# Kernel optimization log

Measured on AMD Instinct MI355X. Metric: run time of the kernel, lower is better.

## Reference

```python
import jax, jax.numpy as jnp
import numpy as np

B, S, D, H = 8, 1024, 1024, 16
HD = D // H
EPS = 1e-06


def setup_inputs() -> dict:
    key = jax.random.key(0)
    ks = jax.random.split(key, 10)
    sc = 0.02
    inp = {
        "y": jax.random.normal(ks[0], (B, S, D), dtype=jnp.float32),
        "y_mask": jax.random.randint(ks[1], (B, 1, 1, S), 0, 2) == 1,
        "Wq": jax.random.normal(ks[2], (D, D), dtype=jnp.float32) * sc,
        "bq": jnp.zeros((D,), jnp.float32),
        "Wk": jax.random.normal(ks[3], (D, D), dtype=jnp.float32) * sc,
        "bk": jnp.zeros((D,), jnp.float32),
        "Wv": jax.random.normal(ks[4], (D, D), dtype=jnp.float32) * sc,
        "bv": jnp.zeros((D,), jnp.float32),
        "Wm": jax.random.normal(ks[5], (D, D), dtype=jnp.float32) * sc,
        "bm": jnp.zeros((D,), jnp.float32),
        "a2": jnp.ones((D,), jnp.float32),
        "b2": jnp.zeros((D,), jnp.float32),
    }
    return inp


def _heads(x):
    # [B,S,D] -> [B,H,S,HD]
    return x.reshape(B, S, H, HD).transpose(0, 2, 1, 3)


def reference(y, y_mask, Wq, bq, Wk, bk, Wv, bv, Wm, bm, a2, b2):
    # torch Linear: x @ W^T + b
    q = _heads(y @ Wq.T + bq)
    k = _heads(y @ Wk.T + bk)
    v = _heads(y @ Wv.T + bv)
    scores = jnp.einsum("bhqd,bhkd->bhqk", q, k) / jnp.sqrt(jnp.float32(HD))
    scores = jnp.where(y_mask, jnp.float32(-1e9), scores)
    att = jax.nn.softmax(scores, axis=-1)  # dropout = identity in eval
    atted = jnp.einsum("bhqk,bhkd->bhqd", att, v)
    atted = atted.transpose(0, 2, 1, 3).reshape(B, S, D)
    atted = atted @ Wm.T + bm
    x = y + atted  # residual (dropout1 = identity in eval)
    mean = x.mean(-1, keepdims=True)
    # torch std: unbiased (ddof=1); eps added to std, not variance
    std = jnp.sqrt(((x - mean) ** 2).sum(-1, keepdims=True) / jnp.float32(D - 1))
    return a2 * (x - mean) / (std + EPS) + b2
```

## Files before the change

### kernel.cpp

```cpp
#include <hip/hip_runtime.h>

#define DEVFN __device__ __forceinline__

typedef unsigned short u16;
typedef __attribute__((ext_vector_type(8))) unsigned short u16x8;
typedef __attribute__((ext_vector_type(4))) unsigned short u16x4;
typedef __attribute__((ext_vector_type(8))) __bf16 bf16x8;
typedef __attribute__((ext_vector_type(4))) float f32x4;

DEVFN u16 f2bf_hw(float f) {
    return __builtin_bit_cast(u16, (__bf16)f);
}

DEVFN float bf2f(u16 h) {
    unsigned u = (unsigned)h << 16;
    return __builtin_bit_cast(float, u);
}

DEVFN bf16x8 ldfrag(const u16* p) {
    return __builtin_bit_cast(bf16x8, *(const u16x8*)p);
}

DEVFN f32x4 mfma16(bf16x8 a, bf16x8 b, f32x4 c) {
    return __builtin_amdgcn_mfma_f32_16x16x32_bf16(a, b, c, 0, 0, 0);
}

DEVFN void async16(const u16* g, u16* l) {
    __builtin_amdgcn_global_load_lds(
        (const __attribute__((address_space(1))) void*)g,
        (__attribute__((address_space(3))) void*)l, 16, 0, 0);
}

__global__ __launch_bounds__(256) void conv_all(const float* __restrict__ y,
                                                const float* __restrict__ w0,
                                                const float* __restrict__ w1,
                                                const float* __restrict__ w2,
                                                const float* __restrict__ w3,
                                                u16* __restrict__ yb,
                                                u16* __restrict__ wb,
                                                const int* __restrict__ mask,
                                                int* __restrict__ idx,
                                                int* __restrict__ cnt) {
    const int b = blockIdx.x;
    if (b >= 12288) {
        const int wave = threadIdx.x >> 6, lane = threadIdx.x & 63;
        for (int bb = wave; bb < 8; bb += 4) {
            const int* m = mask + bb * 1024;
            int* ib = idx + bb * 1024;
            int base = 0;
            for (int t = 0; t < 16; ++t) {
                const int pos = t * 64 + lane;
                const int valid = (m[pos] == 0) ? 1 : 0;
                const unsigned long long bal = __ballot(valid);
                const int pre = __popcll(bal & ((1ull << lane) - 1ull));
                if (valid) ib[base + pre] = pos;
                base += (int)__popcll(bal);
            }
            if (lane == 0) cnt[bb] = base;
            for (int i = base + lane; i < 1024; i += 64) ib[i] = 0;
        }
        return;
    }
    const float* src;
    u16* dst;
    int i;
    if (b < 8192) {
        src = y; dst = yb;
        i = b * 1024 + threadIdx.x * 4;
    } else {
        const int g = (b - 8192) >> 10;
        src = g == 0 ? w0 : (g == 1 ? w1 : (g == 2 ? w2 : w3));
        dst = wb + (size_t)g * 1024 * 1024;
        i = ((b - 8192) & 1023) * 1024 + threadIdx.x * 4;
    }
    const float4 v = *(const float4*)&src[i];
    u16x4 o;
    o.x = f2bf_hw(v.x); o.y = f2bf_hw(v.y);
    o.z = f2bf_hw(v.z); o.w = f2bf_hw(v.w);
    *(u16x4*)&dst[i] = o;
}

__global__ __launch_bounds__(256, 4) void gemm_bt(const u16* __restrict__ A,
                                                  const u16* __restrict__ Bt,
                                                  const float* __restrict__ b0,
                                                  const float* __restrict__ b1,
                                                  const float* __restrict__ b2,
                                                  u16* __restrict__ C0,
                                                  u16* __restrict__ C1,
                                                  u16* __restrict__ C2,
                                                  int K) {
    __shared__ u16 lA[128 * 32];
    __shared__ u16 lB[128 * 32];
    const int tid = threadIdx.x;
    const int wave = tid >> 6, lane = tid & 63;
    const int quad = lane >> 4, l16 = lane & 15;
    const int n0 = blockIdx.x * 128, m0 = blockIdx.y * 128;
    const int wm = (wave >> 1) * 64, wn = (wave & 1) * 64;
    const int srow = tid >> 2, scol = (tid & 3) * 8;
    const u16* Ag0 = A + (size_t)(m0 + srow) * K + scol;
    const u16* Ag1 = A + (size_t)(m0 + 64 + srow) * K + scol;
    const u16* Bg0 = Bt + (size_t)(n0 + srow) * K + scol;
    const u16* Bg1 = Bt + (size_t)(n0 + 64 + srow) * K + scol;
    u16* lA0 = &lA[wave * 512];
    u16* lA1 = &lA[2048 + wave * 512];
    u16* lB0 = &lB[wave * 512];
    u16* lB1 = &lB[2048 + wave * 512];
    f32x4 acc[4][4] = {};
    for (int k0 = 0; k0 < K; k0 += 32) {
        __syncthreads();
        async16(Ag0 + k0, lA0);
        async16(Ag1 + k0, lA1);
        async16(Bg0 + k0, lB0);
        async16(Bg1 + k0, lB1);
        __syncthreads();
        bf16x8 af[4], bfr[4];
        #pragma unroll
        for (int i = 0; i < 4; ++i)
            af[i] = ldfrag(&lA[(wm + i * 16 + l16) * 32 + quad * 8]);
        #pragma unroll
        for (int i = 0; i < 4; ++i)
            bfr[i] = ldfrag(&lB[(wn + i * 16 + l16) * 32 + quad * 8]);
        #pragma unroll
        for (int mi = 0; mi < 4; ++mi)
            #pragma unroll
            for (int ni = 0; ni < 4; ++ni)
                acc[mi][ni] = mfma16(af[mi], bfr[ni], acc[mi][ni]);
    }
    #pragma unroll
    for (int mi = 0; mi < 4; ++mi) {
        #pragma unroll
        for (int ni = 0; ni < 4; ++ni) {
            const int col = n0 + wn + ni * 16 + l16;
            const int cs = col >> 10;
            const int c = col & 1023;
            const float* bp = cs == 0 ? b0 : (cs == 1 ? b1 : b2);
            u16* cp = cs == 0 ? C0 : (cs == 1 ? C1 : C2);
            const float bb = bp[c];
            #pragma unroll
            for (int r = 0; r < 4; ++r) {
                const int row = m0 + wm + mi * 16 + quad * 4 + r;
                cp[(size_t)row * 1024 + c] = f2bf_hw(acc[mi][ni][r] + bb);
            }
        }
    }
}

__global__ __launch_bounds__(256) void transpose_vc(const u16* __restrict__ v,
                                                    u16* __restrict__ vt,
                                                    const int* __restrict__ idx,
                                                    const int* __restrict__ cnt) {
    const int bh = blockIdx.y, bb = bh >> 4, h = bh & 15;
    const int s0 = blockIdx.x * 64;
    const int cn = cnt[bb];
    if (s0 >= ((cn + 63) & ~63)) return;
    __shared__ u16 t[64 * 72];
    const int r = threadIdx.x >> 3, c8 = (threadIdx.x & 7) * 8;
    #pragma unroll
    for (int rr = 0; rr < 64; rr += 32) {
        const int src = idx[bb * 1024 + s0 + r + rr];
        *(u16x8*)&t[(r + rr) * 72 + c8] =
            *(const u16x8*)&v[(size_t)(bb * 1024 + src) * 1024 + h * 64 + c8];
    }
    __syncthreads();
    #pragma unroll
    for (int rr = 0; rr < 64; rr += 32) {
        u16x8 o;
        #pragma unroll
        for (int j = 0; j < 8; ++j) o[j] = t[(c8 + j) * 72 + (r + rr)];
        *(u16x8*)&vt[(size_t)(bh * 64 + r + rr) * 1024 + s0 + c8] = o;
    }
}

__global__ __launch_bounds__(256) void attn(const u16* __restrict__ qb,
                                            const u16* __restrict__ kb,
                                            const u16* __restrict__ vtb,
                                            const int* __restrict__ idxb,
                                            const int* __restrict__ cntb,
                                            u16* __restrict__ attb) {
    const int lin = blockIdx.x;
    const int xcd = lin & 7, slot = lin >> 3;
    const int bh = xcd * 16 + (slot >> 3);
    const int q0 = (slot & 7) * 128;
    const int bb = bh >> 4, h = bh & 15;
    const int tid = threadIdx.x, wave = tid >> 6, lane = tid & 63;
    const int quad = lane >> 4, l16 = lane & 15;
    __shared__ u16 lK[64 * 72];
    __shared__ u16 lV[64 * 72];
    __shared__ u16 lP[128 * 72];

    const int cn = cntb[bb];
    const int kEnd = (cn + 63) & ~63;
    const int* ib = idxb + bb * 1024;

    bf16x8 aq[2][2];
    #pragma unroll
    for (int rg = 0; rg < 2; ++rg) {
        const int qrow = q0 + wave * 32 + rg * 16 + l16;
        const u16* qp = qb + (size_t)(bb * 1024 + qrow) * 1024 + h * 64 + quad * 8;
        aq[rg][0] = ldfrag(qp);
        aq[rg][1] = ldfrag(qp + 32);
    }

    f32x4 o[2][4] = {};
    float ps_acc[2][4] = {};

    const int srow = tid >> 3, scol = (tid & 7) * 8;
    const u16* kbase = kb + (size_t)(bb * 1024) * 1024 + h * 64 + scol;
    const u16* vbase = vtb + (size_t)(bh * 64 + srow) * 1024 + scol;

    int gi0 = ib[srow], gi1 = ib[srow + 32];
    u16x8 nk0 = *(const u16x8*)(kbase + (size_t)gi0 * 1024);
    u16x8 nk1 = *(const u16x8*)(kbase + (size_t)gi1 * 1024);
    u16x8 nv0 = *(const u16x8*)(vbase);
    u16x8 nv1 = *(const u16x8*)(vbase + (size_t)32 * 1024);

    const float C = 0.18033688011112043f;

    for (int kt = 0; kt < kEnd; kt += 64) {
        __syncthreads();
        *(u16x8*)&lK[srow * 72 + scol] = nk0;
        *(u16x8*)&lK[(srow + 32) * 72 + scol] = nk1;
        *(u16x8*)&lV[srow * 72 + scol] = nv0;
        *(u16x8*)&lV[(srow + 32) * 72 + scol] = nv1;
        __syncthreads();
        const int ktn = kt + 64;
        if (ktn < kEnd) {
            gi0 = ib[ktn + srow]; gi1 = ib[ktn + srow + 32];
            nk0 = *(const u16x8*)(kbase + (size_t)gi0 * 1024);
            nk1 = *(const u16x8*)(kbase + (size_t)gi1 * 1024);
            nv0 = *(const u16x8*)(vbase + ktn);
            nv1 = *(const u16x8*)(vbase + (size_t)32 * 1024 + ktn);
        }

        bf16x8 kf[4][2];
        #pragma unroll
        for (int n = 0; n < 4; ++n) {
            kf[n][0] = ldfrag(&lK[(n * 16 + l16) * 72 + quad * 8]);
            kf[n][1] = ldfrag(&lK[(n * 16 + l16) * 72 + 32 + quad * 8]);
        }
        f32x4 s[2][4];
        #pragma unroll
        for (int rg = 0; rg < 2; ++rg)
            #pragma unroll
            for (int n = 0; n < 4; ++n) {
                f32x4 t = {};
                t = mfma16(aq[rg][0], kf[n][0], t);
                t = mfma16(aq[rg][1], kf[n][1], t);
                s[rg][n] = t;
            }
        float bias[4];
        #pragma unroll
        for (int n = 0; n < 4; ++n)
            bias[n] = (kt + n * 16 + l16 < cn) ? 0.0f : -1e9f;
        #pragma unroll
        for (int rg = 0; rg < 2; ++rg)
            #pragma unroll
            for (int n = 0; n < 4; ++n)
                #pragma unroll
                for (int r = 0; r < 4; ++r) {
                    const float p =
                        __builtin_amdgcn_exp2f(__builtin_fmaf(s[rg][n][r], C, bias[n]));
                    ps_acc[rg][r] += p;
                    lP[(wave * 32 + rg * 16 + quad * 4 + r) * 72 + n * 16 + l16] =
                        f2bf_hw(p);
                }
        __asm__ __volatile__("s_waitcnt lgkmcnt(0)" ::: "memory");
        bf16x8 ap[2][2];
        #pragma unroll
        for (int rg = 0; rg < 2; ++rg) {
            ap[rg][0] = ldfrag(&lP[(wave * 32 + rg * 16 + l16) * 72 + quad * 8]);
            ap[rg][1] = ldfrag(&lP[(wave * 32 + rg * 16 + l16) * 72 + 32 + quad * 8]);
        }
        bf16x8 vf[4][2];
        #pragma unroll
        for (int ni = 0; ni < 4; ++ni) {
            vf[ni][0] = ldfrag(&lV[(ni * 16 + l16) * 72 + quad * 8]);
            vf[ni][1] = ldfrag(&lV[(ni * 16 + l16) * 72 + 32 + quad * 8]);
        }
        #pragma unroll
        for (int rg = 0; rg < 2; ++rg)
            #pragma unroll
            for (int ni = 0; ni < 4; ++ni) {
                o[rg][ni] = mfma16(ap[rg][0], vf[ni][0], o[rg][ni]);
                o[rg][ni] = mfma16(ap[rg][1], vf[ni][1], o[rg][ni]);
            }
    }
    #pragma unroll
    for (int off = 1; off < 16; off <<= 1)
        #pragma unroll
        for (int rg = 0; rg < 2; ++rg)
            #pragma unroll
            for (int r = 0; r < 4; ++r)
                ps_acc[rg][r] += __shfl_xor(ps_acc[rg][r], off);
    float rl[2][4];
    #pragma unroll
    for (int rg = 0; rg < 2; ++rg)
        #pragma unroll
        for (int r = 0; r < 4; ++r) rl[rg][r] = 1.f / ps_acc[rg][r];
    #pragma unroll
    for (int rg = 0; rg < 2; ++rg)
        #pragma unroll
        for (int ni = 0; ni < 4; ++ni)
            #pragma unroll
            for (int r = 0; r < 4; ++r) {
                const int row = q0 + wave * 32 + rg * 16 + quad * 4 + r;
                attb[(size_t)(bb * 1024 + row) * 1024 + h * 64 + ni * 16 + l16] =
                    f2bf_hw(o[rg][ni][r] * rl[rg][r]);
            }
}

__global__ __launch_bounds__(256) void ln_res(const float* __restrict__ y,
                                              const u16* __restrict__ xpb,
                                              const float* __restrict__ a2,
                                              const float* __restrict__ b2,
                                              float* __restrict__ out) {
    const int row = blockIdx.x, tid = threadIdx.x;
    const size_t base = (size_t)row * 1024;
    const int j = tid * 4;
    const float4 yv = *(const float4*)&y[base + j];
    const u16x4 xv = *(const u16x4*)&xpb[base + j];
    float x[4] = {yv.x + bf2f(xv.x), yv.y + bf2f(xv.y),
                  yv.z + bf2f(xv.z), yv.w + bf2f(xv.w)};
    float s = 0.f, ss = 0.f;
    #pragma unroll
    for (int i = 0; i < 4; ++i) { s += x[i]; ss += x[i] * x[i]; }
    #pragma unroll
    for (int off = 1; off < 64; off <<= 1) {
        s += __shfl_xor(s, off);
        ss += __shfl_xor(ss, off);
    }
    __shared__ float rs[4], rss[4];
    const int wave = tid >> 6, lane = tid & 63;
    if (lane == 0) { rs[wave] = s; rss[wave] = ss; }
    __syncthreads();
    s = rs[0] + rs[1] + rs[2] + rs[3];
    ss = rss[0] + rss[1] + rss[2] + rss[3];
    const float mean = s * (1.f / 1024.f);
    float var = (ss - s * mean) * (1.f / 1023.f);
    var = fmaxf(var, 0.f);
    const float inv = 1.f / (sqrtf(var) + 1e-6f);
    const float4 av = *(const float4*)&a2[j];
    const float4 bv = *(const float4*)&b2[j];
    float4 ov;
    ov.x = av.x * (x[0] - mean) * inv + bv.x;
    ov.y = av.y * (x[1] - mean) * inv + bv.y;
    ov.z = av.z * (x[2] - mean) * inv + bv.z;
    ov.w = av.w * (x[3] - mean) * inv + bv.w;
    *(float4*)&out[base + j] = ov;
}

extern "C" void kernel_launch(void* const* d_in, const int* in_sizes, int n_in,
                              void* d_out, int out_size, void* d_ws, size_t ws_size,
                              hipStream_t stream) {
    (void)in_sizes; (void)n_in; (void)out_size;
    const float* y   = (const float*)d_in[0];
    const int*   msk = (const int*)d_in[1];
    const float* Wq  = (const float*)d_in[2];
    const float* bq  = (const float*)d_in[3];
    const float* Wk  = (const float*)d_in[4];
    const float* bkb = (const float*)d_in[5];
    const float* Wv  = (const float*)d_in[6];
    const float* bv  = (const float*)d_in[7];
    const float* Wm  = (const float*)d_in[8];
    const float* bm  = (const float*)d_in[9];
    const float* a2  = (const float*)d_in[10];
    const float* b2  = (const float*)d_in[11];
    float* out = (float*)d_out;

    char* ws = (char*)d_ws;
    const size_t MB = 1u << 20;
    if (ws_size < 72 * MB) return;
    u16* yb  = (u16*)(ws);
    u16* wqb = (u16*)(ws + 16 * MB);
    u16* wmb = (u16*)(ws + 22 * MB);
    u16* qb  = (u16*)(ws + 24 * MB);
    u16* kb  = (u16*)(ws + 40 * MB);
    u16* vb  = (u16*)(ws + 56 * MB);
    u16* vtb  = yb;
    u16* attb = vb;
    u16* xpb  = qb;

    int* idxb = (int*)d_out;
    int* cntb = idxb + 8192;

    conv_all<<<12289, 256, 0, stream>>>(y, Wq, Wk, Wv, Wm, yb, wqb,
                                        msk, idxb, cntb);

    gemm_bt<<<dim3(24, 64), 256, 0, stream>>>(
        yb, wqb, bq, bkb, bv, qb, kb, vb, 1024);

    transpose_vc<<<dim3(16, 128), 256, 0, stream>>>(vb, vtb, idxb, cntb);
    attn<<<dim3(1024), 256, 0, stream>>>(qb, kb, vtb, idxb, cntb, attb);

    gemm_bt<<<dim3(8, 64), 256, 0, stream>>>(
        attb, wmb, bm, bm, bm, xpb, xpb, xpb, 1024);
    ln_res<<<8192, 256, 0, stream>>>(y, xpb, a2, b2, out);
}
```

Baseline: 278.1 us.

## Fuse V transpose into attention and split-K the output projection

Removes the standalone V gather/transpose kernel; attention now gathers V rows by index and transposes them into shared memory with scalar stores. The output projection GEMM is split into two K halves to double block count, writing two bf16 partials that the layernorm kernel sums. This trades a kernel launch and a V round-trip through memory for more LDS store work in attention, extra partial-buffer traffic and extra bf16 rounding.

```diff
diff --git a/kernel.cpp b/kernel.cpp
--- a/kernel.cpp
+++ b/kernel.cpp
@@ -88,19 +88,24 @@
                                                   u16* __restrict__ C0,
                                                   u16* __restrict__ C1,
                                                   u16* __restrict__ C2,
-                                                  int K) {
+                                                  u16* __restrict__ Calt,
+                                                  int K, int ld, int nx) {
     __shared__ u16 lA[128 * 32];
     __shared__ u16 lB[128 * 32];
     const int tid = threadIdx.x;
     const int wave = tid >> 6, lane = tid & 63;
     const int quad = lane >> 4, l16 = lane & 15;
-    const int n0 = blockIdx.x * 128, m0 = blockIdx.y * 128;
+    const int bx = blockIdx.x;
+    const int half = bx / nx;
+    const int n0 = (bx % nx) * 128, m0 = blockIdx.y * 128;
     const int wm = (wave >> 1) * 64, wn = (wave & 1) * 64;
     const int srow = tid >> 2, scol = (tid & 3) * 8;
-    const u16* Ag0 = A + (size_t)(m0 + srow) * K + scol;
-    const u16* Ag1 = A + (size_t)(m0 + 64 + srow) * K + scol;
-    const u16* Bg0 = Bt + (size_t)(n0 + srow) * K + scol;
-    const u16* Bg1 = Bt + (size_t)(n0 + 64 + srow) * K + scol;
+    const u16* Ab = A + half * K;
+    const u16* Bb = Bt + half * K;
+    const u16* Ag0 = Ab + (size_t)(m0 + srow) * ld + scol;
+    const u16* Ag1 = Ab + (size_t)(m0 + 64 + srow) * ld + scol;
+    const u16* Bg0 = Bb + (size_t)(n0 + srow) * ld + scol;
+    const u16* Bg1 = Bb + (size_t)(n0 + 64 + srow) * ld + scol;
     u16* lA0 = &lA[wave * 512];
     u16* lA1 = &lA[2048 + wave * 512];
     u16* lB0 = &lB[wave * 512];
@@ -134,8 +139,8 @@
             const int cs = col >> 10;
             const int c = col & 1023;
             const float* bp = cs == 0 ? b0 : (cs == 1 ? b1 : b2);
-            u16* cp = cs == 0 ? C0 : (cs == 1 ? C1 : C2);
-            const float bb = bp[c];
+            u16* cp = half ? Calt : (cs == 0 ? C0 : (cs == 1 ? C1 : C2));
+            const float bb = half ? 0.0f : bp[c];
             #pragma unroll
             for (int r = 0; r < 4; ++r) {
                 const int row = m0 + wm + mi * 16 + quad * 4 + r;
@@ -145,35 +150,9 @@
     }
 }
 
-__global__ __launch_bounds__(256) void transpose_vc(const u16* __restrict__ v,
-                                                    u16* __restrict__ vt,
-                                                    const int* __restrict__ idx,
-                                                    const int* __restrict__ cnt) {
-    const int bh = blockIdx.y, bb = bh >> 4, h = bh & 15;
-    const int s0 = blockIdx.x * 64;
-    const int cn = cnt[bb];
-    if (s0 >= ((cn + 63) & ~63)) return;
-    __shared__ u16 t[64 * 72];
-    const int r = threadIdx.x >> 3, c8 = (threadIdx.x & 7) * 8;
-    #pragma unroll
-    for (int rr = 0; rr < 64; rr += 32) {
-        const int src = idx[bb * 1024 + s0 + r + rr];
-        *(u16x8*)&t[(r + rr) * 72 + c8] =
-            *(const u16x8*)&v[(size_t)(bb * 1024 + src) * 1024 + h * 64 + c8];
-    }
-    __syncthreads();
-    #pragma unroll
-    for (int rr = 0; rr < 64; rr += 32) {
-        u16x8 o;
-        #pragma unroll
-        for (int j = 0; j < 8; ++j) o[j] = t[(c8 + j) * 72 + (r + rr)];
-        *(u16x8*)&vt[(size_t)(bh * 64 + r + rr) * 1024 + s0 + c8] = o;
-    }
-}
-
 __global__ __launch_bounds__(256) void attn(const u16* __restrict__ qb,
                                             const u16* __restrict__ kb,
-                                            const u16* __restrict__ vtb,
+                                            const u16* __restrict__ vb,
                                             const int* __restrict__ idxb,
                                             const int* __restrict__ cntb,
                                             u16* __restrict__ attb) {
@@ -206,13 +185,13 @@
 
     const int srow = tid >> 3, scol = (tid & 7) * 8;
     const u16* kbase = kb + (size_t)(bb * 1024) * 1024 + h * 64 + scol;
-    const u16* vbase = vtb + (size_t)(bh * 64 + srow) * 1024 + scol;
+    const u16* vbase = vb + (size_t)(bb * 1024) * 1024 + h * 64 + scol;
 
     int gi0 = ib[srow], gi1 = ib[srow + 32];
     u16x8 nk0 = *(const u16x8*)(kbase + (size_t)gi0 * 1024);
     u16x8 nk1 = *(const u16x8*)(kbase + (size_t)gi1 * 1024);
-    u16x8 nv0 = *(const u16x8*)(vbase);
-    u16x8 nv1 = *(const u16x8*)(vbase + (size_t)32 * 1024);
+    u16x8 nv0 = *(const u16x8*)(vbase + (size_t)gi0 * 1024);
+    u16x8 nv1 = *(const u16x8*)(vbase + (size_t)gi1 * 1024);
 
     const float C = 0.18033688011112043f;
 
@@ -220,16 +199,19 @@
         __syncthreads();
         *(u16x8*)&lK[srow * 72 + scol] = nk0;
         *(u16x8*)&lK[(srow + 32) * 72 + scol] = nk1;
-        *(u16x8*)&lV[srow * 72 + scol] = nv0;
-        *(u16x8*)&lV[(srow + 32) * 72 + scol] = nv1;
+        #pragma unroll
+        for (int j = 0; j < 8; ++j) {
+            lV[(scol + j) * 72 + srow] = nv0[j];
+            lV[(scol + j) * 72 + srow + 32] = nv1[j];
+        }
         __syncthreads();
         const int ktn = kt + 64;
         if (ktn < kEnd) {
             gi0 = ib[ktn + srow]; gi1 = ib[ktn + srow + 32];
             nk0 = *(const u16x8*)(kbase + (size_t)gi0 * 1024);
             nk1 = *(const u16x8*)(kbase + (size_t)gi1 * 1024);
-            nv0 = *(const u16x8*)(vbase + ktn);
-            nv1 = *(const u16x8*)(vbase + (size_t)32 * 1024 + ktn);
+            nv0 = *(const u16x8*)(vbase + (size_t)gi0 * 1024);
+            nv1 = *(const u16x8*)(vbase + (size_t)gi1 * 1024);
         }
 
         bf16x8 kf[4][2];
@@ -310,7 +292,8 @@
 }
 
 __global__ __launch_bounds__(256) void ln_res(const float* __restrict__ y,
-                                              const u16* __restrict__ xpb,
+                                              const u16* __restrict__ xp0,
+                                              const u16* __restrict__ xp1,
                                               const float* __restrict__ a2,
                                               const float* __restrict__ b2,
                                               float* __restrict__ out) {
@@ -318,9 +301,12 @@
     const size_t base = (size_t)row * 1024;
     const int j = tid * 4;
     const float4 yv = *(const float4*)&y[base + j];
-    const u16x4 xv = *(const u16x4*)&xpb[base + j];
-    float x[4] = {yv.x + bf2f(xv.x), yv.y + bf2f(xv.y),
-                  yv.z + bf2f(xv.z), yv.w + bf2f(xv.w)};
+    const u16x4 x0 = *(const u16x4*)&xp0[base + j];
+    const u16x4 x1 = *(const u16x4*)&xp1[base + j];
+    float x[4] = {yv.x + bf2f(x0.x) + bf2f(x1.x),
+                  yv.y + bf2f(x0.y) + bf2f(x1.y),
+                  yv.z + bf2f(x0.z) + bf2f(x1.z),
+                  yv.w + bf2f(x0.w) + bf2f(x1.w)};
     float s = 0.f, ss = 0.f;
     #pragma unroll
     for (int i = 0; i < 4; ++i) { s += x[i]; ss += x[i] * x[i]; }
@@ -376,9 +362,9 @@
     u16* qb  = (u16*)(ws + 24 * MB);
     u16* kb  = (u16*)(ws + 40 * MB);
     u16* vb  = (u16*)(ws + 56 * MB);
-    u16* vtb  = yb;
-    u16* attb = vb;
-    u16* xpb  = qb;
+    u16* attb = yb;
+    u16* xp0  = qb;
+    u16* xp1  = kb;
 
     int* idxb = (int*)d_out;
     int* cntb = idxb + 8192;
@@ -387,12 +373,12 @@
                                         msk, idxb, cntb);
 
     gemm_bt<<<dim3(24, 64), 256, 0, stream>>>(
-        yb, wqb, bq, bkb, bv, qb, kb, vb, 1024);
-
-    transpose_vc<<<dim3(16, 128), 256, 0, stream>>>(vb, vtb, idxb, cntb);
-    attn<<<dim3(1024), 256, 0, stream>>>(qb, kb, vtb, idxb, cntb, attb);
-
-    gemm_bt<<<dim3(8, 64), 256, 0, stream>>>(
-        attb, wmb, bm, bm, bm, xpb, xpb, xpb, 1024);
-    ln_res<<<8192, 256, 0, stream>>>(y, xpb, a2, b2, out);
-}
+        yb, wqb, bq, bkb, bv, qb, kb, vb, vb, 1024, 1024, 24);
+
+    attn<<<dim3(1024), 256, 0, stream>>>(qb, kb, vb, idxb, cntb, attb);
+
+    gemm_bt<<<dim3(16, 64), 256, 0, stream>>>(
+        attb, wmb, bm, bm, bm, xp0, xp0, xp0, xp1, 512, 1024, 8);
+
+    ln_res<<<8192, 256, 0, stream>>>(y, xp0, xp1, a2, b2, out);
+}
```

Measured after the change: 292.8 us. 1.05x slower.
